# Performance work log

Measured on AMD Instinct MI355X. Metric: run time of the kernel, lower is better.

The kernel has to match this reference:

```python
import jax, jax.numpy as jnp
import numpy as np

B, S, D = 2, 2048, 1024
H = 16
DK = D // H
DFF = 4096
EPS = 1e-6


def rotate_half(x):
    x1, x2 = jnp.split(x, 2, axis=-1)
    return jnp.concatenate((-x2, x1), axis=-1)


def build_rope(dim, seq_len):
    inv_freq = 1.0 / (10000.0 ** (jnp.arange(0, dim, 2, dtype=jnp.float32) / dim))
    t = jnp.arange(seq_len, dtype=jnp.float32)
    freqs = jnp.einsum('i,j->ij', t, inv_freq)
    emb = jnp.concatenate((freqs, freqs), axis=-1)
    return jnp.cos(emb)[None, None], jnp.sin(emb)[None, None]  # [1,1,S,dk]


def rmsnorm(x, g):
    rms = jnp.sqrt(jnp.mean(x * x, axis=-1, keepdims=True) + EPS)
    return x / rms * g


def setup_inputs() -> dict:
    key = jax.random.key(0)
    ks = jax.random.split(key, 10)
    sc = 0.02
    x = jax.random.normal(ks[0], (B, S, D), dtype=jnp.float32)
    mask = jnp.tril(jnp.ones((S, S), dtype=jnp.int32))[None, None]  # causal [1,1,S,S]
    wq = jax.random.normal(ks[1], (D, D), dtype=jnp.float32) * sc
    wk = jax.random.normal(ks[2], (D, D), dtype=jnp.float32) * sc
    wv = jax.random.normal(ks[3], (D, D), dtype=jnp.float32) * sc
    wo = jax.random.normal(ks[4], (D, D), dtype=jnp.float32) * sc
    w1 = jax.random.normal(ks[5], (2 * DFF, D), dtype=jnp.float32) * sc
    w2 = jax.random.normal(ks[6], (D, DFF), dtype=jnp.float32) * sc
    g1 = jnp.ones((D,), dtype=jnp.float32)
    g2 = jnp.ones((D,), dtype=jnp.float32)
    return {"x": x, "mask": mask, "wq": wq, "wk": wk, "wv": wv, "wo": wo,
            "w1": w1, "w2": w2, "g1": g1, "g2": g2}


def decoder_block(x, mask, wq, wk, wv, wo, w1, w2, g1, g2):
    b, s, d = x.shape
    # --- self-attention sublayer ---
    h = rmsnorm(x, g1)
    q = (h @ wq.T).reshape(b, s, H, DK).transpose(0, 2, 1, 3)
    k = (h @ wk.T).reshape(b, s, H, DK).transpose(0, 2, 1, 3)
    v = (h @ wv.T).reshape(b, s, H, DK).transpose(0, 2, 1, 3)
    cos, sin = build_rope(DK, s)
    q = q * cos + rotate_half(q) * sin
    k = k * cos + rotate_half(k) * sin
    scores = jnp.einsum('bhqd,bhkd->bhqk', q, k) / jnp.sqrt(jnp.float32(DK))
    scores = jnp.where(mask == 0, jnp.float32(-1e9), scores)
    p = jax.nn.softmax(scores, axis=-1)
    ctx = jnp.einsum('bhqk,bhkd->bhqd', p, v)
    ctx = ctx.transpose(0, 2, 1, 3).reshape(b, s, d)
    x = x + ctx @ wo.T
    # --- SwiGLU FFN sublayer ---
    h2 = rmsnorm(x, g2)
    u = h2 @ w1.T  # [b,s,2*DFF]
    u1, u2 = jnp.split(u, 2, axis=-1)
    ffn = (u1 * jax.nn.silu(u2)) @ w2.T
    return x + ffn


def reference(x, mask, wq, wk, wv, wo, w1, w2, g1, g2):
    return decoder_block(x, mask, wq, wk, wv, wo, w1, w2, g1, g2)
```

## Files before the change

### kernel.cpp

```cpp
#include <hip/hip_runtime.h>
#include <hip/hip_bf16.h>

#define BB 2
#define SS 2048
#define DD 1024
#define NH 16
#define DKH 64
#define DFF 4096
#define MTOK (BB*SS)

typedef __hip_bfloat16 bf16;
typedef __attribute__((ext_vector_type(8))) short s16x8;
typedef __attribute__((ext_vector_type(4))) float f32x4;

__device__ __forceinline__ float bs2f(short s) {
    unsigned int u = ((unsigned int)(unsigned short)s) << 16;
    return __uint_as_float(u);
}
__device__ __forceinline__ float b2f(bf16 v) { return __bfloat162float(v); }
__device__ __forceinline__ bf16 f2b(float v) { return __float2bfloat16(v); }
__device__ __forceinline__ short f2bs(float v) {
    bf16 b = __float2bfloat16(v);
    return *(short*)&b;
}

__device__ __forceinline__ void load16(const bf16* g, bf16* l) {
    __builtin_amdgcn_global_load_lds((const __attribute__((address_space(1))) void*)g,
                                     (__attribute__((address_space(3))) void*)l,
                                     16, 0, 0);
}

#define WAITV(N) asm volatile("s_waitcnt vmcnt(" #N ")" ::: "memory")


__global__ void cvt_kernel(const float* __restrict__ src, bf16* __restrict__ dst) {
    const int i = blockIdx.x * blockDim.x + threadIdx.x;
    float4 v = ((const float4*)src)[i];
    short4 o;
    o.x = f2bs(v.x); o.y = f2bs(v.y); o.z = f2bs(v.z); o.w = f2bs(v.w);
    ((short4*)dst)[i] = o;
}

__global__ void cvt4_kernel(const float* __restrict__ s0, const float* __restrict__ s1,
                            const float* __restrict__ s2, const float* __restrict__ s3,
                            bf16* __restrict__ dst) {
    const int z = blockIdx.z;
    const float* src = (z == 0) ? s0 : (z == 1) ? s1 : (z == 2) ? s2 : s3;
    const int i = blockIdx.x * blockDim.x + threadIdx.x;
    float4 v = ((const float4*)src)[i];
    short4 o;
    o.x = f2bs(v.x); o.y = f2bs(v.y); o.z = f2bs(v.z); o.w = f2bs(v.w);
    ((short4*)(dst + (size_t)z * DD * DD))[i] = o;
}

__global__ void rmsnorm_kernel(const float* __restrict__ x, const float* __restrict__ g,
                               bf16* __restrict__ out) {
    const int row = blockIdx.x;
    const int tid = threadIdx.x;
    float4 xv = ((const float4*)(x + (size_t)row * DD))[tid];
    float ss = xv.x*xv.x + xv.y*xv.y + xv.z*xv.z + xv.w*xv.w;
    #pragma unroll
    for (int off = 32; off > 0; off >>= 1) ss += __shfl_down(ss, off);
    __shared__ float red[4];
    const int wv = tid >> 6, lane = tid & 63;
    if (lane == 0) red[wv] = ss;
    __syncthreads();
    const float tot = red[0] + red[1] + red[2] + red[3];
    const float inv = rsqrtf(tot * (1.0f / DD) + 1e-6f);
    float4 gv = ((const float4*)g)[tid];
    short4 o;
    o.x = f2bs(xv.x * inv * gv.x);
    o.y = f2bs(xv.y * inv * gv.y);
    o.z = f2bs(xv.z * inv * gv.z);
    o.w = f2bs(xv.w * inv * gv.w);
    ((short4*)(out + (size_t)row * DD))[tid] = o;
}

__global__ __launch_bounds__(256) void gemm_qkv(const bf16* __restrict__ A,
                                                const bf16* __restrict__ Wbase,
                                                bf16* __restrict__ Obase) {
    __shared__ bf16 As[128 * 32];
    __shared__ bf16 Bs[128 * 32];
    const int tid = threadIdx.x, lane = tid & 63, wv = tid >> 6;
    const int col = lane & 15, quad = lane >> 4;
    const int wm = wv >> 1, wn = wv & 1;
    const int m0 = blockIdx.y * 128;
    const int n0 = blockIdx.x * 128;
    const bf16* W = Wbase + (size_t)blockIdx.z * DD * DD;
    bf16* C = Obase + (size_t)blockIdx.z * MTOK * DD;

    const int srow = tid >> 2;
    const int scol = (((tid & 3) ^ (srow & 3))) * 8;
    const bf16* Ag = A + (size_t)(m0 + srow) * DD + scol;
    const bf16* Wg = W + (size_t)(n0 + srow) * DD + scol;
    bf16* Asl = As + tid * 8;
    bf16* Bsl = Bs + tid * 8;
    const size_t half = (size_t)64 * DD;
    const int rg = (quad ^ (col & 3)) * 8;

    f32x4 acc[4][4] = {};
    for (int k0 = 0; k0 < DD; k0 += 32) {
        __syncthreads();
        load16(Ag + k0,        Asl);
        load16(Ag + half + k0, Asl + 2048);
        load16(Wg + k0,        Bsl);
        load16(Wg + half + k0, Bsl + 2048);
        __syncthreads();
        s16x8 af[4], bfr[4];
        #pragma unroll
        for (int t = 0; t < 4; t++) {
            af[t]  = *(const s16x8*)(As + (wm * 64 + t * 16 + col) * 32 + rg);
            bfr[t] = *(const s16x8*)(Bs + (wn * 64 + t * 16 + col) * 32 + rg);
        }
        #pragma unroll
        for (int tm = 0; tm < 4; tm++)
            #pragma unroll
            for (int tn = 0; tn < 4; tn++)
                acc[tm][tn] = __builtin_amdgcn_mfma_f32_16x16x32_bf16(af[tm], bfr[tn], acc[tm][tn], 0, 0, 0);
    }
    #pragma unroll
    for (int tm = 0; tm < 4; tm++)
        #pragma unroll
        for (int tn = 0; tn < 4; tn++)
            #pragma unroll
            for (int r = 0; r < 4; r++) {
                const int rr = m0 + wm * 64 + tm * 16 + quad * 4 + r;
                const int cc = n0 + wn * 64 + tn * 16 + col;
                C[(size_t)rr * DD + cc] = f2b(acc[tm][tn][r]);
            }
}

__global__ __launch_bounds__(256) void gemm128_atomic(const bf16* __restrict__ A,
                                                      const bf16* __restrict__ W,
                                                      float* C, int N, int K, int KC) {
    __shared__ bf16 As[128 * 32];
    __shared__ bf16 Bs[128 * 32];
    const int tid = threadIdx.x, lane = tid & 63, wv = tid >> 6;
    const int col = lane & 15, quad = lane >> 4;
    const int wm = wv >> 1, wn = wv & 1;
    const int m0 = blockIdx.y * 128;
    const int n0 = blockIdx.x * 128;
    const int koff = blockIdx.z * KC;

    const int srow = tid >> 2;
    const int scol = (((tid & 3) ^ (srow & 3))) * 8;
    const bf16* Ag = A + (size_t)(m0 + srow) * K + scol;
    const bf16* Wg = W + (size_t)(n0 + srow) * K + scol;
    bf16* Asl = As + tid * 8;
    bf16* Bsl = Bs + tid * 8;
    const size_t half = (size_t)64 * K;
    const int rg = (quad ^ (col & 3)) * 8;

    f32x4 acc[4][4] = {};
    for (int k0 = koff; k0 < koff + KC; k0 += 32) {
        __syncthreads();
        load16(Ag + k0,        Asl);
        load16(Ag + half + k0, Asl + 2048);
        load16(Wg + k0,        Bsl);
        load16(Wg + half + k0, Bsl + 2048);
        __syncthreads();
        s16x8 af[4], bfr[4];
        #pragma unroll
        for (int t = 0; t < 4; t++) {
            af[t]  = *(const s16x8*)(As + (wm * 64 + t * 16 + col) * 32 + rg);
            bfr[t] = *(const s16x8*)(Bs + (wn * 64 + t * 16 + col) * 32 + rg);
        }
        #pragma unroll
        for (int tm = 0; tm < 4; tm++)
            #pragma unroll
            for (int tn = 0; tn < 4; tn++)
                acc[tm][tn] = __builtin_amdgcn_mfma_f32_16x16x32_bf16(af[tm], bfr[tn], acc[tm][tn], 0, 0, 0);
    }
    #pragma unroll
    for (int tm = 0; tm < 4; tm++)
        #pragma unroll
        for (int tn = 0; tn < 4; tn++)
            #pragma unroll
            for (int r = 0; r < 4; r++) {
                const int rr = m0 + wm * 64 + tm * 16 + quad * 4 + r;
                const int cc = n0 + wn * 64 + tn * 16 + col;
                atomicAdd(&C[(size_t)rr * N + cc], acc[tm][tn][r]);
            }
}

__global__ __launch_bounds__(256) void gemm64n_f32res(const bf16* __restrict__ A,
                                                      const bf16* __restrict__ W,
                                                      const float* res, float* C,
                                                      int M, int N, int K) {
    __shared__ bf16 As[128 * 32];
    __shared__ bf16 Bs[64 * 32];
    const int tid = threadIdx.x, lane = tid & 63, wv = tid >> 6;
    const int col = lane & 15, quad = lane >> 4;
    const int wm = wv >> 1, wn = wv & 1;
    const int m0 = blockIdx.y * 128;
    const int n0 = blockIdx.x * 64;

    const int srow = tid >> 2;
    const int scol = (((tid & 3) ^ (srow & 3))) * 8;
    const bf16* Ag = A + (size_t)(m0 + srow) * K + scol;
    const bf16* Wg = W + (size_t)(n0 + srow) * K + scol;
    bf16* Asl = As + tid * 8;
    bf16* Bsl = Bs + tid * 8;
    const size_t half = (size_t)64 * K;
    const int rg = (quad ^ (col & 3)) * 8;

    f32x4 acc[4][2] = {};
    for (int k0 = 0; k0 < K; k0 += 32) {
        __syncthreads();
        load16(Ag + k0,        Asl);
        load16(Ag + half + k0, Asl + 2048);
        load16(Wg + k0,        Bsl);
        __syncthreads();
        s16x8 af[4], bfr[2];
        #pragma unroll
        for (int t = 0; t < 4; t++)
            af[t] = *(const s16x8*)(As + (wm * 64 + t * 16 + col) * 32 + rg);
        #pragma unroll
        for (int t = 0; t < 2; t++)
            bfr[t] = *(const s16x8*)(Bs + (wn * 32 + t * 16 + col) * 32 + rg);
        #pragma unroll
        for (int tm = 0; tm < 4; tm++)
            #pragma unroll
            for (int tn = 0; tn < 2; tn++)
                acc[tm][tn] = __builtin_amdgcn_mfma_f32_16x16x32_bf16(af[tm], bfr[tn], acc[tm][tn], 0, 0, 0);
    }
    #pragma unroll
    for (int tm = 0; tm < 4; tm++)
        #pragma unroll
        for (int tn = 0; tn < 2; tn++)
            #pragma unroll
            for (int r = 0; r < 4; r++) {
                const int rr = m0 + wm * 64 + tm * 16 + quad * 4 + r;
                const int cc = n0 + wn * 32 + tn * 16 + col;
                C[(size_t)rr * N + cc] = acc[tm][tn][r] + res[(size_t)rr * N + cc];
            }
}

__device__ __forceinline__ void stage_k32(const bf16* Ag, const bf16* Wg0,
                                          const bf16* Wg1, bf16* Abuf, bf16* Bbuf,
                                          int k0, int tid) {
    load16(Ag + k0,                    Abuf + tid * 8);
    load16(Ag + (size_t)128 * DD + k0, Abuf + tid * 8 + 4096);
    load16(Wg0 + k0,                   Bbuf + tid * 8);
    load16(Wg1 + k0,                   Bbuf + tid * 8 + 4096);
}

__device__ __forceinline__ void comp_k32(const bf16* Ap, const bf16* Bp,
                                         f32x4 (*acc)[4],
                                         int wm, int wn, int col, int quad) {
    const int rg = (quad ^ (col & 3)) * 8;
    s16x8 af[8], bfr[4];
    #pragma unroll
    for (int t = 0; t < 8; t++)
        af[t] = *(const s16x8*)(Ap + (wm * 128 + t * 16 + col) * 32 + rg);
    #pragma unroll
    for (int t = 0; t < 4; t++)
        bfr[t] = *(const s16x8*)(Bp + (wn * 64 + t * 16 + col) * 32 + rg);
    __builtin_amdgcn_s_setprio(1);
    #pragma unroll
    for (int tm = 0; tm < 8; tm++)
        #pragma unroll
        for (int tn = 0; tn < 4; tn++)
            acc[tm][tn] = __builtin_amdgcn_mfma_f32_16x16x32_bf16(af[tm], bfr[tn], acc[tm][tn], 0, 0, 0);
    __builtin_amdgcn_s_setprio(0);
}

__global__ __launch_bounds__(512, 2) void gemm256_swiglu(const bf16* __restrict__ A,
                                                         const bf16* __restrict__ W,
                                                         bf16* __restrict__ G) {
    __shared__ bf16 As[4][256 * 32];
    __shared__ bf16 Bs[4][256 * 32];
    const int tid = threadIdx.x, lane = tid & 63, wv = tid >> 6;
    const int col = lane & 15, quad = lane >> 4;
    const int wm = wv >> 2, wn = wv & 3;
    const int m0 = blockIdx.y * 256;
    const int n0 = blockIdx.x * 128;

    const int srow = tid >> 2;
    const int scol = ((tid & 3) ^ (srow & 3)) * 8;
    const bf16* Ag = A + (size_t)(m0 + srow) * DD + scol;
    const int r0 = srow, r1 = srow + 128;
    const int wr0 = n0 + ((r0 >> 6) << 5) + (r0 & 31) + (((r0 >> 5) & 1) ? DFF : 0);
    const int wr1 = n0 + ((r1 >> 6) << 5) + (r1 & 31) + (((r1 >> 5) & 1) ? DFF : 0);
    const bf16* Wg0 = W + (size_t)wr0 * DD + scol;
    const bf16* Wg1 = W + (size_t)wr1 * DD + scol;

    f32x4 acc[8][4] = {};

    stage_k32(Ag, Wg0, Wg1, As[0], Bs[0], 0,  tid);
    stage_k32(Ag, Wg0, Wg1, As[1], Bs[1], 32, tid);
    stage_k32(Ag, Wg0, Wg1, As[2], Bs[2], 64, tid);

    for (int t = 0; t < 29; t++) {
        WAITV(8);
        __builtin_amdgcn_s_barrier();
        asm volatile("" ::: "memory");
        stage_k32(Ag, Wg0, Wg1, As[(t + 3) & 3], Bs[(t + 3) & 3], (t + 3) * 32, tid);
        comp_k32(As[t & 3], Bs[t & 3], acc, wm, wn, col, quad);
    }
    WAITV(8);
    __builtin_amdgcn_s_barrier();
    asm volatile("" ::: "memory");
    comp_k32(As[29 & 3], Bs[29 & 3], acc, wm, wn, col, quad);
    WAITV(4);
    __builtin_amdgcn_s_barrier();
    asm volatile("" ::: "memory");
    comp_k32(As[30 & 3], Bs[30 & 3], acc, wm, wn, col, quad);
    WAITV(0);
    __builtin_amdgcn_s_barrier();
    asm volatile("" ::: "memory");
    comp_k32(As[31 & 3], Bs[31 & 3], acc, wm, wn, col, quad);

    #pragma unroll
    for (int tm = 0; tm < 8; tm++)
        #pragma unroll
        for (int tn = 0; tn < 2; tn++)
            #pragma unroll
            for (int r = 0; r < 4; r++) {
                const int rr = m0 + wm * 128 + tm * 16 + quad * 4 + r;
                const int cc = n0 + wn * 32 + tn * 16 + col;
                const float u1 = acc[tm][tn][r];
                const float u2 = acc[tm][tn + 2][r];
                const float sig = 1.0f / (1.0f + __expf(-u2));
                G[(size_t)rr * DFF + cc] = f2b(u1 * u2 * sig);
            }
}

__global__ void rope_kernel(bf16* __restrict__ q, bf16* __restrict__ k) {
    const int idx = blockIdx.x * blockDim.x + threadIdx.x;
    const int d = idx & 31;
    const int h = (idx >> 5) & (NH - 1);
    const int row = idx >> 9;
    const int s = row & (SS - 1);
    const float invf = powf(10000.0f, -(float)d * (1.0f / 32.0f));
    const float ang = (float)s * invf;
    float sn, cs;
    sincosf(ang, &sn, &cs);
    const size_t base = (size_t)row * DD + h * DKH + d;
    {
        float x1 = b2f(q[base]), x2 = b2f(q[base + 32]);
        q[base]      = f2b(x1 * cs - x2 * sn);
        q[base + 32] = f2b(x2 * cs + x1 * sn);
    }
    {
        float x1 = b2f(k[base]), x2 = b2f(k[base + 32]);
        k[base]      = f2b(x1 * cs - x2 * sn);
        k[base + 32] = f2b(x2 * cs + x1 * sn);
    }
}

__global__ __launch_bounds__(256) void vt_transpose(const bf16* __restrict__ v,
                                                    bf16* __restrict__ vt) {
    __shared__ short tile[64][72];
    const int s0 = blockIdx.x * 64;
    const int bh = blockIdx.y;
    const int b = bh >> 4, h = bh & 15;
    const bf16* src = v + (size_t)b * SS * DD + h * DKH;
    #pragma unroll
    for (int it = 0; it < 2; it++) {
        const int sl = (threadIdx.x >> 3) + it * 32;
        const int dp = (threadIdx.x & 7) * 8;
        s16x8 val = *(const s16x8*)(src + (size_t)(s0 + sl) * DD + dp);
        *(s16x8*)&tile[sl][dp] = val;
    }
    __syncthreads();
    bf16* dst = vt + (size_t)bh * DKH * SS;
    #pragma unroll
    for (int it = 0; it < 2; it++) {
        const int dk = (threadIdx.x >> 3) + it * 32;
        const int sp = (threadIdx.x & 7) * 8;
        s16x8 o;
        #pragma unroll
        for (int j = 0; j < 8; j++) o[j] = tile[sp + j][dk];
        *(s16x8*)(dst + (size_t)dk * SS + s0 + sp) = o;
    }
}

__device__ __forceinline__ void stage_kv(const bf16* kbase, const bf16* vtbase,
                                         bf16* Kd, bf16* Vd, int kt0, int tid) {
    const int row0 = tid >> 3;
    const int gl = tid & 7;
    #pragma unroll
    for (int r = 0; r < 2; r++) {
        const int row = row0 + r * 32;
        const int g = (gl ^ (row & 7)) * 8;
        load16(kbase + (size_t)(kt0 + row) * DD + g, Kd + tid * 8 + r * 2048);
        load16(vtbase + (size_t)row * SS + kt0 + g,  Vd + tid * 8 + r * 2048);
    }
}

__device__ __forceinline__ void attn_step(const bf16* Ks, const bf16* Vs,
                                          short (*pl)[72],
                                          s16x8 qf0, s16x8 qf1,
                                          f32x4* cacc, float* lacc,
                                          int col, int quad, int kt0, int q0w,
                                          bool need_mask) {
    f32x4 s4[4] = {};
    #pragma unroll
    for (int t = 0; t < 4; t++) {
        const int key = 16 * t + col;
        const int g0 = (quad ^ (key & 7)) * 8;
        s16x8 b0 = *(const s16x8*)(Ks + key * 64 + g0);
        s16x8 b1 = *(const s16x8*)(Ks + key * 64 + (g0 ^ 32));
        s4[t] = __builtin_amdgcn_mfma_f32_16x16x32_bf16(qf0, b0, s4[t], 0, 0, 0);
        s4[t] = __builtin_amdgcn_mfma_f32_16x16x32_bf16(qf1, b1, s4[t], 0, 0, 0);
    }
    #pragma unroll
    for (int t = 0; t < 4; t++)
        #pragma unroll
        for (int r = 0; r < 4; r++) {
            float sv = s4[t][r] * 0.125f;
            if (need_mask) {
                const int key = kt0 + 16 * t + col;
                const int qq  = q0w + quad * 4 + r;
                if (key > qq) sv = -1.0e30f;
            }
            const float p = __expf(sv);
            s4[t][r] = p;
            lacc[r] += p;
        }
    #pragma unroll
    for (int t = 0; t < 4; t++)
        #pragma unroll
        for (int r = 0; r < 4; r++)
            pl[quad * 4 + r][col + 16 * t] = f2bs(s4[t][r]);
    s16x8 pf0 = *(const s16x8*)&pl[col][quad * 8];
    s16x8 pf1 = *(const s16x8*)&pl[col][32 + quad * 8];
    #pragma unroll
    for (int tn = 0; tn < 4; tn++) {
        const int dk = 16 * tn + col;
        const int g0 = (quad ^ (dk & 7)) * 8;
        s16x8 b0 = *(const s16x8*)(Vs + dk * 64 + g0);
        s16x8 b1 = *(const s16x8*)(Vs + dk * 64 + (g0 ^ 32));
        cacc[tn] = __builtin_amdgcn_mfma_f32_16x16x32_bf16(pf0, b0, cacc[tn], 0, 0, 0);
        cacc[tn] = __builtin_amdgcn_mfma_f32_16x16x32_bf16(pf1, b1, cacc[tn], 0, 0, 0);
    }
}

__global__ __launch_bounds__(256) void attn_mfma2(const bf16* __restrict__ q,
                                                  const bf16* __restrict__ k,
                                                  const bf16* __restrict__ vt,
                                                  bf16* __restrict__ ctx) {
    __shared__ bf16 Ks[2][64 * 64];
    __shared__ bf16 Vs[2][64 * 64];
    __shared__ short plds[4][16][72];
    const int tid = threadIdx.x, lane = tid & 63, wv = tid >> 6;
    const int col = lane & 15, quad = lane >> 4;
    const int bh = blockIdx.y;
    const int b = bh >> 4, h = bh & 15;
    const int tA = blockIdx.x;
    const int tB = 31 - tA;
    const int q0A = tA * 64 + wv * 16;
    const int q0B = tB * 64 + wv * 16;

    const bf16* kbase  = k  + (size_t)b * SS * DD + h * DKH;
    const bf16* vtbase = vt + (size_t)bh * DKH * SS;

    const bf16* qrA = q + (size_t)(b * SS + q0A + col) * DD + h * DKH + quad * 8;
    const bf16* qrB = q + (size_t)(b * SS + q0B + col) * DD + h * DKH + quad * 8;
    s16x8 qfA0 = *(const s16x8*)(qrA);
    s16x8 qfA1 = *(const s16x8*)(qrA + 32);
    s16x8 qfB0 = *(const s16x8*)(qrB);
    s16x8 qfB1 = *(const s16x8*)(qrB + 32);

    f32x4 caccA[4] = {}, caccB[4] = {};
    float lA[4] = {}, lB[4] = {};

    const int last = tB;
    stage_kv(kbase, vtbase, Ks[0], Vs[0], 0, tid);
    int buf = 0;
    for (int kt = 0; kt <= last; kt++) {
        __syncthreads();
        if (kt < last)
            stage_kv(kbase, vtbase, Ks[buf ^ 1], Vs[buf ^ 1], (kt + 1) * 64, tid);
        const bf16* Kc = Ks[buf];
        const bf16* Vc = Vs[buf];
        if (kt <= tA)
            attn_step(Kc, Vc, plds[wv], qfA0, qfA1, caccA, lA,
                      col, quad, kt * 64, q0A, kt == tA);
        attn_step(Kc, Vc, plds[wv], qfB0, qfB1, caccB, lB,
                  col, quad, kt * 64, q0B, kt == tB);
        buf ^= 1;
    }
    #pragma unroll
    for (int r = 0; r < 4; r++) {
        #pragma unroll
        for (int off = 1; off < 16; off <<= 1) {
            lA[r] += __shfl_xor(lA[r], off);
            lB[r] += __shfl_xor(lB[r], off);
        }
    }
    #pragma unroll
    for (int tn = 0; tn < 4; tn++)
        #pragma unroll
        for (int r = 0; r < 4; r++) {
            const size_t tokA = (size_t)(b * SS + q0A + quad * 4 + r);
            ctx[tokA * DD + h * DKH + 16 * tn + col] = f2b(caccA[tn][r] / lA[r]);
            const size_t tokB = (size_t)(b * SS + q0B + quad * 4 + r);
            ctx[tokB * DD + h * DKH + 16 * tn + col] = f2b(caccB[tn][r] / lB[r]);
        }
}

extern "C" void kernel_launch(void* const* d_in, const int* in_sizes, int n_in,
                              void* d_out, int out_size, void* d_ws, size_t ws_size,
                              hipStream_t stream) {
    const float* x  = (const float*)d_in[0];
    const float* wq = (const float*)d_in[2];
    const float* wk = (const float*)d_in[3];
    const float* wv = (const float*)d_in[4];
    const float* wo = (const float*)d_in[5];
    const float* w1 = (const float*)d_in[6];
    const float* w2 = (const float*)d_in[7];
    const float* g1 = (const float*)d_in[8];
    const float* g2 = (const float*)d_in[9];
    float* out = (float*)d_out;
    char* ws = (char*)d_ws;

    const size_t MB = 1024 * 1024;
    bf16* hb   = (bf16*)(ws + 0 * MB);
    bf16* qb   = (bf16*)(ws + 8 * MB);
    bf16* kb   = (bf16*)(ws + 16 * MB);
    bf16* vb   = (bf16*)(ws + 24 * MB);
    bf16* ctxb = hb;
    bf16* h2b  = hb;
    bf16* gb   = qb;
    bf16* wqb  = (bf16*)(ws + 32 * MB);
    bf16* wob  = wqb + (size_t)3 * DD * DD;
    bf16* vtb  = (bf16*)(ws + 40 * MB);
    bf16* w1b  = (bf16*)(ws + 40 * MB);
    bf16* w2b  = (bf16*)(ws + 56 * MB);

    cvt4_kernel<<<dim3((DD * DD / 4) / 256, 1, 4), 256, 0, stream>>>(
        wq, wk, wv, wo, wqb);

    rmsnorm_kernel<<<MTOK, 256, 0, stream>>>(x, g1, hb);
    gemm_qkv<<<dim3(DD / 128, MTOK / 128, 3), 256, 0, stream>>>(hb, wqb, qb);

    vt_transpose<<<dim3(SS / 64, BB * NH), 256, 0, stream>>>(vb, vtb);
    rope_kernel<<<(BB * SS * NH * 32) / 256, 256, 0, stream>>>(qb, kb);

    attn_mfma2<<<dim3(16, BB * NH), 256, 0, stream>>>(qb, kb, vtb, ctxb);

    gemm64n_f32res<<<dim3(DD / 64, MTOK / 128), 256, 0, stream>>>(
        ctxb, wob, x, out, MTOK, DD, DD);
    rmsnorm_kernel<<<MTOK, 256, 0, stream>>>(out, g2, h2b);

    cvt_kernel<<<(2 * DFF * DD / 4) / 256, 256, 0, stream>>>(w1, w1b);
    cvt_kernel<<<(DD * DFF / 4) / 256, 256, 0, stream>>>(w2, w2b);

    gemm256_swiglu<<<dim3(DFF / 128, MTOK / 256), 512, 0, stream>>>(h2b, w1b, gb);
    gemm128_atomic<<<dim3(DD / 128, MTOK / 128, 2), 256, 0, stream>>>(
        gb, w2b, out, DD, DFF, DFF / 2);
}
```

Measured before the change: 449.6 us.

## Restructure SwiGLU GEMM mainloop into 8-wave ping-pong double-buffered schedule

```diff
diff --git a/kernel.cpp b/kernel.cpp
--- a/kernel.cpp
+++ b/kernel.cpp
@@ -236,40 +236,29 @@
             }
 }
 
-__device__ __forceinline__ void stage_k32(const bf16* Ag, const bf16* Wg0,
-                                          const bf16* Wg1, bf16* Abuf, bf16* Bbuf,
-                                          int k0, int tid) {
-    load16(Ag + k0,                    Abuf + tid * 8);
-    load16(Ag + (size_t)128 * DD + k0, Abuf + tid * 8 + 4096);
-    load16(Wg0 + k0,                   Bbuf + tid * 8);
-    load16(Wg1 + k0,                   Bbuf + tid * 8 + 4096);
-}
-
-__device__ __forceinline__ void comp_k32(const bf16* Ap, const bf16* Bp,
-                                         f32x4 (*acc)[4],
-                                         int wm, int wn, int col, int quad) {
-    const int rg = (quad ^ (col & 3)) * 8;
-    s16x8 af[8], bfr[4];
-    #pragma unroll
-    for (int t = 0; t < 8; t++)
-        af[t] = *(const s16x8*)(Ap + (wm * 128 + t * 16 + col) * 32 + rg);
+__device__ __forceinline__ void rd4(const bf16* P, int base, int col, int rg,
+                                    s16x8* a) {
     #pragma unroll
     for (int t = 0; t < 4; t++)
-        bfr[t] = *(const s16x8*)(Bp + (wn * 64 + t * 16 + col) * 32 + rg);
+        a[t] = *(const s16x8*)(P + (base + t * 16 + col) * 32 + rg);
+}
+
+__device__ __forceinline__ void mfma4x4(const s16x8* a, const s16x8* b,
+                                        f32x4 (*acc)[4], int mo) {
     __builtin_amdgcn_s_setprio(1);
     #pragma unroll
-    for (int tm = 0; tm < 8; tm++)
-        #pragma unroll
-        for (int tn = 0; tn < 4; tn++)
-            acc[tm][tn] = __builtin_amdgcn_mfma_f32_16x16x32_bf16(af[tm], bfr[tn], acc[tm][tn], 0, 0, 0);
+    for (int i = 0; i < 4; i++)
+        #pragma unroll
+        for (int j = 0; j < 4; j++)
+            acc[mo + i][j] = __builtin_amdgcn_mfma_f32_16x16x32_bf16(a[i], b[j], acc[mo + i][j], 0, 0, 0);
     __builtin_amdgcn_s_setprio(0);
 }
 
 __global__ __launch_bounds__(512, 2) void gemm256_swiglu(const bf16* __restrict__ A,
                                                          const bf16* __restrict__ W,
                                                          bf16* __restrict__ G) {
-    __shared__ bf16 As[4][256 * 32];
-    __shared__ bf16 Bs[4][256 * 32];
+    __shared__ bf16 As[2][2][256 * 32];
+    __shared__ bf16 Bs[2][2][256 * 32];
     const int tid = threadIdx.x, lane = tid & 63, wv = tid >> 6;
     const int col = lane & 15, quad = lane >> 4;
     const int wm = wv >> 2, wn = wv & 3;
@@ -285,31 +274,80 @@
     const bf16* Wg0 = W + (size_t)wr0 * DD + scol;
     const bf16* Wg1 = W + (size_t)wr1 * DD + scol;
 
+    const int rg = (quad ^ (col & 3)) * 8;
+    const int am0 = wm * 128;
+    const int am1 = wm * 128 + 64;
+    const int bb  = wn * 64;
+
     f32x4 acc[8][4] = {};
 
-    stage_k32(Ag, Wg0, Wg1, As[0], Bs[0], 0,  tid);
-    stage_k32(Ag, Wg0, Wg1, As[1], Bs[1], 32, tid);
-    stage_k32(Ag, Wg0, Wg1, As[2], Bs[2], 64, tid);
-
-    for (int t = 0; t < 29; t++) {
-        WAITV(8);
-        __builtin_amdgcn_s_barrier();
-        asm volatile("" ::: "memory");
-        stage_k32(Ag, Wg0, Wg1, As[(t + 3) & 3], Bs[(t + 3) & 3], (t + 3) * 32, tid);
-        comp_k32(As[t & 3], Bs[t & 3], acc, wm, wn, col, quad);
-    }
-    WAITV(8);
-    __builtin_amdgcn_s_barrier();
-    asm volatile("" ::: "memory");
-    comp_k32(As[29 & 3], Bs[29 & 3], acc, wm, wn, col, quad);
+    auto stageA = [&](int buf, int kh, int k0) {
+        bf16* P = &As[buf][kh][0];
+        load16(Ag + k0,                    P + tid * 8);
+        load16(Ag + (size_t)128 * DD + k0, P + tid * 8 + 4096);
+    };
+    auto stageB = [&](int buf, int kh, int k0) {
+        bf16* P = &Bs[buf][kh][0];
+        load16(Wg0 + k0, P + tid * 8);
+        load16(Wg1 + k0, P + tid * 8 + 4096);
+    };
+
+    stageA(0, 0, 0);
+    stageB(0, 0, 0);
+    stageA(0, 1, 32);
+    stageB(0, 1, 32);
     WAITV(4);
     __builtin_amdgcn_s_barrier();
-    asm volatile("" ::: "memory");
-    comp_k32(As[30 & 3], Bs[30 & 3], acc, wm, wn, col, quad);
-    WAITV(0);
-    __builtin_amdgcn_s_barrier();
-    asm volatile("" ::: "memory");
-    comp_k32(As[31 & 3], Bs[31 & 3], acc, wm, wn, col, quad);
+
+    for (int t = 0; t < 15; t++) {
+        const int buf = t & 1, nb = buf ^ 1;
+        const int kn = (t + 1) * 64;
+        s16x8 a[4], b0[4], b1[4];
+
+        rd4(&As[buf][0][0], am0, col, rg, a);
+        rd4(&Bs[buf][0][0], bb,  col, rg, b0);
+        stageA(nb, 0, kn);
+        __builtin_amdgcn_s_barrier();
+        mfma4x4(a, b0, acc, 0);
+        __builtin_amdgcn_s_barrier();
+
+        rd4(&As[buf][0][0], am1, col, rg, a);
+        stageB(nb, 0, kn);
+        __builtin_amdgcn_s_barrier();
+        mfma4x4(a, b0, acc, 4);
+        WAITV(4);
+        __builtin_amdgcn_s_barrier();
+
+        rd4(&As[buf][1][0], am0, col, rg, a);
+        rd4(&Bs[buf][1][0], bb,  col, rg, b1);
+        stageA(nb, 1, kn + 32);
+        __builtin_amdgcn_s_barrier();
+        mfma4x4(a, b1, acc, 0);
+        __builtin_amdgcn_s_barrier();
+
+        rd4(&As[buf][1][0], am1, col, rg, a);
+        stageB(nb, 1, kn + 32);
+        __builtin_amdgcn_s_barrier();
+        mfma4x4(a, b1, acc, 4);
+        WAITV(4);
+        __builtin_amdgcn_s_barrier();
+    }
+    {
+        s16x8 a[4], b0[4], b1[4];
+        rd4(&As[1][0][0], am0, col, rg, a);
+        rd4(&Bs[1][0][0], bb,  col, rg, b0);
+        __builtin_amdgcn_s_barrier();
+        mfma4x4(a, b0, acc, 0);
+        rd4(&As[1][0][0], am1, col, rg, a);
+        mfma4x4(a, b0, acc, 4);
+        WAITV(0);
+        __builtin_amdgcn_s_barrier();
+        rd4(&As[1][1][0], am0, col, rg, a);
+        rd4(&Bs[1][1][0], bb,  col, rg, b1);
+        mfma4x4(a, b1, acc, 0);
+        rd4(&As[1][1][0], am1, col, rg, a);
+        mfma4x4(a, b1, acc, 4);
+    }
 
     #pragma unroll
     for (int tm = 0; tm < 8; tm++)
```

After: 447.6 us. About the same (-0.4%).
